# Kernel tuning notes

Measured on AMD Instinct MI355X. Metric: run time of the kernel, lower is better.

## Reference

```python
import jax, jax.numpy as jnp
from jax import lax
import numpy as np

# 32 branches: 14 base features + (worker,agv,box) x 2 entities x (state,task,pose)
DIMS = [10,3,2,3,2,8,6,8,6,3,2,2,1,1, 7,11,12, 7,11,12, 4,7,10, 4,7,10, 3,4,10, 3,4,10]
N_BRANCH = 32   # == len(VectorizedEmbedding.state_types)
T = 2048        # torch LSTM sees 2-D input as an unbatched sequence of length 'batch'
H = 256         # hidden_size
E = 2 * H       # bidirectional feature dim (d_model for attention)
DMAX = 12       # max per-branch input dim; inputs/weights zero-padded to this
NHEAD = 4


def setup_inputs() -> dict:
    key = jax.random.key(0)
    ks = jax.random.split(key, 16)
    s = 0.1
    x = jax.random.normal(ks[0], (N_BRANCH, T, DMAX), jnp.float32)
    mask = np.zeros((N_BRANCH, 1, DMAX), np.float32)
    for i, d in enumerate(DIMS):
        mask[i, 0, :d] = 1.0
    x = x * jnp.asarray(mask)  # zero padding -> identical math to per-branch dims
    inp = {
        'x': x,
        'w_ih_f': jax.random.normal(ks[1], (N_BRANCH, 4 * H, DMAX), jnp.float32) * s,
        'w_hh_f': jax.random.normal(ks[2], (N_BRANCH, 4 * H, H), jnp.float32) * s,
        'b_f':    jax.random.normal(ks[3], (N_BRANCH, 4 * H), jnp.float32) * s,
        'w_ih_b': jax.random.normal(ks[4], (N_BRANCH, 4 * H, DMAX), jnp.float32) * s,
        'w_hh_b': jax.random.normal(ks[5], (N_BRANCH, 4 * H, H), jnp.float32) * s,
        'b_b':    jax.random.normal(ks[6], (N_BRANCH, 4 * H), jnp.float32) * s,
        'type_emb': jax.random.normal(ks[7], (N_BRANCH, E), jnp.float32) * s,
        'wq': jax.random.normal(ks[8], (E, E), jnp.float32) * s,
        'bq': jnp.zeros((E,), jnp.float32),
        'wk': jax.random.normal(ks[9], (E, E), jnp.float32) * s,
        'bk': jnp.zeros((E,), jnp.float32),
        'wv': jax.random.normal(ks[10], (E, E), jnp.float32) * s,
        'bv': jnp.zeros((E,), jnp.float32),
        'wo': jax.random.normal(ks[11], (E, E), jnp.float32) * s,
        'bo': jnp.zeros((E,), jnp.float32),
    }
    return inp


def _lstm_dir(x, w_ih, w_hh, b):
    # x: (N,T,D); w_ih: (N,4H,D); w_hh: (N,4H,H); b: (N,4H) (= b_ih + b_hh)
    xw = jnp.einsum('ntd,ngd->ntg', x, w_ih) + b[:, None, :]  # (N,T,4H)
    h0 = jnp.zeros((x.shape[0], w_hh.shape[-1]), x.dtype)

    def step(carry, xt):
        h, c = carry
        g = xt + jnp.einsum('nh,ngh->ng', h, w_hh)
        i, f, gg, o = jnp.split(g, 4, axis=-1)  # torch gate order i,f,g,o
        c = jax.nn.sigmoid(f) * c + jax.nn.sigmoid(i) * jnp.tanh(gg)
        h = jax.nn.sigmoid(o) * jnp.tanh(c)
        return (h, c), h

    _, hs = lax.scan(step, (h0, h0), jnp.swapaxes(xw, 0, 1))  # hs: (T,N,H)
    return jnp.swapaxes(hs, 0, 1)  # (N,T,H)


def _forward(x, w_ih_f, w_hh_f, b_f, w_ih_b, w_hh_b, b_b, type_emb,
             wq, bq, wk, bk, wv, bv, wo, bo):
    fwd = _lstm_dir(x, w_ih_f, w_hh_f, b_f)
    bwd = _lstm_dir(x[:, ::-1], w_ih_b, w_hh_b, b_b)[:, ::-1]
    embs = jnp.concatenate([fwd, bwd], axis=-1)      # (N,T,E)
    all_embs = jnp.swapaxes(embs, 0, 1)              # (T,N,E) == (batch, seq, d_model)

    # MultiheadAttentionGlobalHead: q = slot 0, k = inputs + type_embedding, v = inputs
    B = all_embs.shape[0]
    d = E // NHEAD
    q = all_embs[:, 0] @ wq.T + bq                   # (B,E)
    k = (all_embs + type_emb[None]) @ wk.T + bk      # (B,N,E)
    v = all_embs @ wv.T + bv                         # (B,N,E)
    qh = q.reshape(B, NHEAD, d)
    kh = k.reshape(B, N_BRANCH, NHEAD, d)
    vh = v.reshape(B, N_BRANCH, NHEAD, d)
    scores = jnp.einsum('bhd,bshd->bhs', qh, kh) / jnp.sqrt(jnp.float32(d))
    w = jax.nn.softmax(scores, axis=-1)              # (B,H,S); dropout off (eval)
    ctx = jnp.einsum('bhs,bshd->bhd', w, vh).reshape(B, E)
    out = ctx @ wo.T + bo                            # (B,E)
    attn = w.mean(axis=1)                            # (B,S) avg over heads (torch default)
    return out, attn


def reference(x, w_ih_f, w_hh_f, b_f, w_ih_b, w_hh_b, b_b, type_emb,
              wq, bq, wk, bk, wv, bv, wo, bo):
    return _forward(x, w_ih_f, w_hh_f, b_f, w_ih_b, w_hh_b, b_b, type_emb,
                    wq, bq, wk, bk, wv, bv, wo, bo)
```

## Files before the change

kernel.cpp:

```cpp
#include <hip/hip_runtime.h>

typedef _Float16 half_t;
typedef _Float16 half2_t __attribute__((ext_vector_type(2)));
typedef _Float16 half4_t __attribute__((ext_vector_type(4)));
typedef _Float16 half8_t __attribute__((ext_vector_type(8)));
typedef float    floatx4 __attribute__((ext_vector_type(4)));

#define T_SEQ 2048
#define EDIM  512

static constexpr size_t EMB_OFF = 0;
static constexpr size_t Q_OFF   = 67108864;
static constexpr size_t WQ_OFF  = Q_OFF  + 2097152;
static constexpr size_t WK_OFF  = WQ_OFF + 524288;
static constexpr size_t WV_OFF  = WK_OFF + 524288;
static constexpr size_t WO_OFF  = WV_OFF + 524288;
static constexpr size_t TE_OFF  = WO_OFF + 524288;

__device__ __forceinline__ float fdot2f(half2_t a, half2_t b, float c) {
#if __has_builtin(__builtin_amdgcn_fdot2)
  return __builtin_amdgcn_fdot2(a, b, c, false);
#else
  return c + (float)a[0] * (float)b[0] + (float)a[1] * (float)b[1];
#endif
}
__device__ __forceinline__ half2_t mkh2(float a, float b) {
  half2_t r; r[0] = (half_t)a; r[1] = (half_t)b; return r;
}
__device__ __forceinline__ half2_t h2bc(unsigned u) { return __builtin_bit_cast(half2_t, u); }
__device__ __forceinline__ unsigned h2u(half2_t h)  { return __builtin_bit_cast(unsigned, h); }
__device__ __forceinline__ float sigm(float v)  { return __builtin_amdgcn_rcpf(1.f + __expf(-v)); }
__device__ __forceinline__ float tanhf_(float v){ return __builtin_amdgcn_rcpf(1.f + __expf(-2.f * v)) * 2.f - 1.f; }

__global__ void convert_kernel(const float* __restrict__ wq, const float* __restrict__ wk,
                               const float* __restrict__ wvv, const float* __restrict__ wo,
                               const float* __restrict__ te, const float* __restrict__ x,
                               half_t* __restrict__ wq16, half_t* __restrict__ wk16,
                               half_t* __restrict__ wv16, half_t* __restrict__ wo16,
                               half_t* __restrict__ te16, half_t* __restrict__ x16) {
  int i4 = (blockIdx.x * 256 + threadIdx.x) * 4;
  const float* src; half_t* dst; int off;
  if      (i4 < 262144)     { src = wq;  dst = wq16; off = i4; }
  else if (i4 < 2 * 262144) { src = wk;  dst = wk16; off = i4 - 262144; }
  else if (i4 < 3 * 262144) { src = wvv; dst = wv16; off = i4 - 2 * 262144; }
  else if (i4 < 4 * 262144) { src = wo;  dst = wo16; off = i4 - 3 * 262144; }
  else if (i4 < 4 * 262144 + 16384) { src = te; dst = te16; off = i4 - 4 * 262144; }
  else                      { src = x;   dst = x16;  off = i4 - (4 * 262144 + 16384); }
  float4 v = *(const float4*)(src + off);
  half4_t h; h[0] = (half_t)v.x; h[1] = (half_t)v.y; h[2] = (half_t)v.z; h[3] = (half_t)v.w;
  *(half4_t*)(dst + off) = h;
}

#define HB_STRIDE 272
#define LSTM_LDS_BYTES (16 * 512 * 16 + 2 * HB_STRIDE * 2)

__global__ __launch_bounds__(512, 1)
void lstm_kernel(const half_t* __restrict__ x16,
                 const float* __restrict__ wih_f, const float* __restrict__ whh_f, const float* __restrict__ b_f,
                 const float* __restrict__ wih_b, const float* __restrict__ whh_b, const float* __restrict__ b_b,
                 half_t* __restrict__ emb) {
  extern __shared__ char smem[];
  uint4*  wtail = (uint4*)smem;
  half_t* hbuf  = (half_t*)(smem + 16 * 512 * 16);

  const int bid = blockIdx.x;
  const int n = bid >> 1, dir = bid & 1;
  const int t = threadIdx.x;
  const int j = t >> 1, hf = t & 1;
  const float* wih  = dir ? wih_b : wih_f;
  const float* whh  = dir ? whh_b : whh_f;
  const float* bias = dir ? b_b   : b_f;

  half2_t w[4][48];
  half2_t wir[2][6];
  float   bb0, bb1;

#pragma unroll
  for (int r = 0; r < 4; ++r) {
    const size_t row = (size_t)n * 1024 + r * 256 + j;
    const float4* wp = (const float4*)(whh + row * 256 + hf * 128);
#pragma unroll
    for (int c = 0; c < 24; ++c) {
      float4 w4 = wp[c];
      w[r][c * 2]     = mkh2(w4.x, w4.y);
      w[r][c * 2 + 1] = mkh2(w4.z, w4.w);
    }
#pragma unroll
    for (int c = 0; c < 4; ++c) {
      float4 a = wp[24 + 2 * c], b2 = wp[25 + 2 * c];
      uint4 u;
      u.x = h2u(mkh2(a.x, a.y));   u.y = h2u(mkh2(a.z, a.w));
      u.z = h2u(mkh2(b2.x, b2.y)); u.w = h2u(mkh2(b2.z, b2.w));
      wtail[(r * 4 + c) * 512 + t] = u;
    }
  }
  {
    const int rbase = hf * 2;
#pragma unroll
    for (int rr = 0; rr < 2; ++rr) {
      const size_t row = (size_t)n * 1024 + (rbase + rr) * 256 + j;
      const float4* ip = (const float4*)(wih + row * 12);
      float4 a = ip[0], b2 = ip[1], c4 = ip[2];
      wir[rr][0] = mkh2(a.x, a.y);  wir[rr][1] = mkh2(a.z, a.w);
      wir[rr][2] = mkh2(b2.x, b2.y); wir[rr][3] = mkh2(b2.z, b2.w);
      wir[rr][4] = mkh2(c4.x, c4.y); wir[rr][5] = mkh2(c4.z, c4.w);
    }
    bb0 = bias[(size_t)n * 1024 + (rbase + 0) * 256 + j];
    bb1 = bias[(size_t)n * 1024 + (rbase + 1) * 256 + j];
  }
  if (t < 2 * HB_STRIDE) hbuf[t] = (half_t)0.f;
  __syncthreads();

  float cst = 0.f;
  half2_t xh[6];
  {
    const int t0 = dir ? 2047 : 0;
    const uint2* xp = (const uint2*)(x16 + ((size_t)n * T_SEQ + t0) * 12);
    uint2 u0 = xp[0], u1 = xp[1], u2 = xp[2];
    xh[0] = h2bc(u0.x); xh[1] = h2bc(u0.y);
    xh[2] = h2bc(u1.x); xh[3] = h2bc(u1.y);
    xh[4] = h2bc(u2.x); xh[5] = h2bc(u2.y);
  }

#pragma unroll 1
  for (int s = 0; s < T_SEQ; ++s) {
    const int tcur = dir ? (2047 - s) : s;
    int tnext = dir ? (2046 - s) : (s + 1);
    if (s == 2047) tnext = tcur;

    float p0 = bb0, p1 = bb1;
#pragma unroll
    for (int d = 0; d < 6; ++d) {
      p0 = fdot2f(wir[0][d], xh[d], p0);
      p1 = fdot2f(wir[1][d], xh[d], p1);
    }

    {
      const uint2* xnp = (const uint2*)(x16 + ((size_t)n * T_SEQ + tnext) * 12);
      uint2 u0 = xnp[0], u1 = xnp[1], u2 = xnp[2];
      xh[0] = h2bc(u0.x); xh[1] = h2bc(u0.y);
      xh[2] = h2bc(u1.x); xh[3] = h2bc(u1.y);
      xh[4] = h2bc(u2.x); xh[5] = h2bc(u2.y);
    }

    float acc0 = hf ? 0.f : p0;
    float acc1 = hf ? 0.f : p1;
    float acc2 = hf ? p0 : 0.f;
    float acc3 = hf ? p1 : 0.f;

    const uint4* hb = (const uint4*)(hbuf + (s & 1) * HB_STRIDE) + hf * 17;
#pragma unroll
    for (int c = 0; c < 12; ++c) {
      uint4 hv = hb[c];
      half2_t h0 = h2bc(hv.x), h1 = h2bc(hv.y), h2 = h2bc(hv.z), h3 = h2bc(hv.w);
      acc0 = fdot2f(w[0][4 * c + 0], h0, acc0);
      acc0 = fdot2f(w[0][4 * c + 1], h1, acc0);
      acc0 = fdot2f(w[0][4 * c + 2], h2, acc0);
      acc0 = fdot2f(w[0][4 * c + 3], h3, acc0);
      acc1 = fdot2f(w[1][4 * c + 0], h0, acc1);
      acc1 = fdot2f(w[1][4 * c + 1], h1, acc1);
      acc1 = fdot2f(w[1][4 * c + 2], h2, acc1);
      acc1 = fdot2f(w[1][4 * c + 3], h3, acc1);
      acc2 = fdot2f(w[2][4 * c + 0], h0, acc2);
      acc2 = fdot2f(w[2][4 * c + 1], h1, acc2);
      acc2 = fdot2f(w[2][4 * c + 2], h2, acc2);
      acc2 = fdot2f(w[2][4 * c + 3], h3, acc2);
      acc3 = fdot2f(w[3][4 * c + 0], h0, acc3);
      acc3 = fdot2f(w[3][4 * c + 1], h1, acc3);
      acc3 = fdot2f(w[3][4 * c + 2], h2, acc3);
      acc3 = fdot2f(w[3][4 * c + 3], h3, acc3);
    }
#pragma unroll
    for (int c = 0; c < 4; ++c) {
      uint4 hv = hb[12 + c];
      half2_t h0 = h2bc(hv.x), h1 = h2bc(hv.y), h2 = h2bc(hv.z), h3 = h2bc(hv.w);
      uint4 w0 = wtail[(0 * 4 + c) * 512 + t];
      acc0 = fdot2f(h2bc(w0.x), h0, acc0);
      acc0 = fdot2f(h2bc(w0.y), h1, acc0);
      acc0 = fdot2f(h2bc(w0.z), h2, acc0);
      acc0 = fdot2f(h2bc(w0.w), h3, acc0);
      uint4 w1 = wtail[(1 * 4 + c) * 512 + t];
      acc1 = fdot2f(h2bc(w1.x), h0, acc1);
      acc1 = fdot2f(h2bc(w1.y), h1, acc1);
      acc1 = fdot2f(h2bc(w1.z), h2, acc1);
      acc1 = fdot2f(h2bc(w1.w), h3, acc1);
      uint4 w2 = wtail[(2 * 4 + c) * 512 + t];
      acc2 = fdot2f(h2bc(w2.x), h0, acc2);
      acc2 = fdot2f(h2bc(w2.y), h1, acc2);
      acc2 = fdot2f(h2bc(w2.z), h2, acc2);
      acc2 = fdot2f(h2bc(w2.w), h3, acc2);
      uint4 w3 = wtail[(3 * 4 + c) * 512 + t];
      acc3 = fdot2f(h2bc(w3.x), h0, acc3);
      acc3 = fdot2f(h2bc(w3.y), h1, acc3);
      acc3 = fdot2f(h2bc(w3.z), h2, acc3);
      acc3 = fdot2f(h2bc(w3.w), h3, acc3);
    }

    acc0 += __shfl_xor(acc0, 1);
    acc1 += __shfl_xor(acc1, 1);
    acc2 += __shfl_xor(acc2, 1);
    acc3 += __shfl_xor(acc3, 1);

    float si = sigm(acc0), sf = sigm(acc1), gg = tanhf_(acc2), so = sigm(acc3);
    cst = sf * cst + si * gg;
    float h = so * tanhf_(cst);
    if (!hf) {
      half_t hh = (half_t)h;
      const int pos = j + ((j >> 7) << 3);
      hbuf[((s + 1) & 1) * HB_STRIDE + pos] = hh;
      emb[((size_t)n * T_SEQ + tcur) * EDIM + dir * 256 + j] = hh;
    }
    __syncthreads();
  }
}

__global__ __launch_bounds__(256, 1)
void qproj_kernel(const half_t* __restrict__ emb, const half_t* __restrict__ wq16,
                  const float* __restrict__ bq, half_t* __restrict__ q_ws) {
  const int t0 = blockIdx.x * 32;
  const int tid = threadIdx.x;
  const int lane = tid & 63, wid = tid >> 6;
  const int col = lane & 15, grp = lane >> 4;

  floatx4 acc[2][8];
#pragma unroll
  for (int nt = 0; nt < 8; ++nt) {
    int eo = wid * 128 + nt * 16 + col;
    float b = bq[eo];
#pragma unroll
    for (int mt = 0; mt < 2; ++mt) { acc[mt][nt][0] = b; acc[mt][nt][1] = b; acc[mt][nt][2] = b; acc[mt][nt][3] = b; }
  }
  for (int kc = 0; kc < 16; ++kc) {
    const int e = kc * 32 + grp * 8;
    half8_t a[2];
#pragma unroll
    for (int mt = 0; mt < 2; ++mt) {
      int trow = t0 + mt * 16 + col;
      a[mt] = *(const half8_t*)(emb + (size_t)trow * EDIM + e);
    }
#pragma unroll
    for (int nt = 0; nt < 8; ++nt) {
      int eo = wid * 128 + nt * 16 + col;
      half8_t bf = *(const half8_t*)(wq16 + (size_t)eo * EDIM + e);
#pragma unroll
      for (int mt = 0; mt < 2; ++mt)
        acc[mt][nt] = __builtin_amdgcn_mfma_f32_16x16x32_f16(a[mt], bf, acc[mt][nt], 0, 0, 0);
    }
  }
#pragma unroll
  for (int mt = 0; mt < 2; ++mt)
#pragma unroll
    for (int nt = 0; nt < 8; ++nt)
#pragma unroll
      for (int r = 0; r < 4; ++r) {
        int trow = t0 + mt * 16 + grp * 4 + r;
        int eo = wid * 128 + nt * 16 + col;
        q_ws[(size_t)trow * EDIM + eo] = (half_t)acc[mt][nt][r];
      }
}

__global__ __launch_bounds__(256, 1)
void attn_kernel(const half_t* __restrict__ emb, const half_t* __restrict__ q_ws,
                 const half_t* __restrict__ wk16, const half_t* __restrict__ wv16,
                 const half_t* __restrict__ wo16, const half_t* __restrict__ te16,
                 const float* __restrict__ bk, const float* __restrict__ bv,
                 const float* __restrict__ bo, float* __restrict__ out) {
  __shared__ float  scores_lds[128];
  __shared__ float  w_lds[128];
  __shared__ half_t ctx_lds[512];

  const int t = blockIdx.x;
  const int tid = threadIdx.x;
  const int lane = tid & 63, wid = tid >> 6;
  const int col = lane & 15, grp = lane >> 4;

  floatx4 kacc[2][8], vacc[2][8];
#pragma unroll
  for (int nt = 0; nt < 8; ++nt) {
    int eo = wid * 128 + nt * 16 + col;
    float kb = bk[eo], vb = bv[eo];
#pragma unroll
    for (int mt = 0; mt < 2; ++mt) {
      kacc[mt][nt][0] = kb; kacc[mt][nt][1] = kb; kacc[mt][nt][2] = kb; kacc[mt][nt][3] = kb;
      vacc[mt][nt][0] = vb; vacc[mt][nt][1] = vb; vacc[mt][nt][2] = vb; vacc[mt][nt][3] = vb;
    }
  }
  for (int kc = 0; kc < 16; ++kc) {
    const int e = kc * 32 + grp * 8;
    half8_t av[2], ak[2];
#pragma unroll
    for (int mt = 0; mt < 2; ++mt) {
      int branch = mt * 16 + col;
      av[mt] = *(const half8_t*)(emb + ((size_t)branch * T_SEQ + t) * EDIM + e);
      half8_t te = *(const half8_t*)(te16 + (size_t)branch * EDIM + e);
      ak[mt] = av[mt] + te;
    }
#pragma unroll
    for (int nt = 0; nt < 8; ++nt) {
      int eo = wid * 128 + nt * 16 + col;
      half8_t bkf = *(const half8_t*)(wk16 + (size_t)eo * EDIM + e);
      half8_t bvf = *(const half8_t*)(wv16 + (size_t)eo * EDIM + e);
#pragma unroll
      for (int mt = 0; mt < 2; ++mt) {
        kacc[mt][nt] = __builtin_amdgcn_mfma_f32_16x16x32_f16(ak[mt], bkf, kacc[mt][nt], 0, 0, 0);
        vacc[mt][nt] = __builtin_amdgcn_mfma_f32_16x16x32_f16(av[mt], bvf, vacc[mt][nt], 0, 0, 0);
      }
    }
  }

  float spart[8];
#pragma unroll
  for (int i = 0; i < 8; ++i) spart[i] = 0.f;
#pragma unroll
  for (int nt = 0; nt < 8; ++nt) {
    int eo = wid * 128 + nt * 16 + col;
    float qf = (float)q_ws[(size_t)t * EDIM + eo];
#pragma unroll
    for (int mt = 0; mt < 2; ++mt)
#pragma unroll
      for (int r = 0; r < 4; ++r)
        spart[mt * 4 + r] += qf * kacc[mt][nt][r];
  }
#pragma unroll
  for (int i = 0; i < 8; ++i) {
    float v = spart[i];
    v += __shfl_xor(v, 1); v += __shfl_xor(v, 2); v += __shfl_xor(v, 4); v += __shfl_xor(v, 8);
    spart[i] = v;
  }
  const float scale = 0.08838834764831845f;
  if (col == 0) {
#pragma unroll
    for (int mt = 0; mt < 2; ++mt)
#pragma unroll
      for (int r = 0; r < 4; ++r)
        scores_lds[wid * 32 + mt * 16 + grp * 4 + r] = spart[mt * 4 + r] * scale;
  }
  float sc = scores_lds[wid * 32 + (lane & 31)];
  float m = sc;
  m = fmaxf(m, __shfl_xor(m, 1));  m = fmaxf(m, __shfl_xor(m, 2));
  m = fmaxf(m, __shfl_xor(m, 4));  m = fmaxf(m, __shfl_xor(m, 8));
  m = fmaxf(m, __shfl_xor(m, 16));
  float ex = __expf(sc - m);
  float sm = ex;
  sm += __shfl_xor(sm, 1); sm += __shfl_xor(sm, 2); sm += __shfl_xor(sm, 4);
  sm += __shfl_xor(sm, 8); sm += __shfl_xor(sm, 16);
  float wn = ex * __builtin_amdgcn_rcpf(sm);
  if (lane < 32) w_lds[wid * 32 + lane] = wn;

  float wb[8];
#pragma unroll
  for (int mt = 0; mt < 2; ++mt)
#pragma unroll
    for (int r = 0; r < 4; ++r)
      wb[mt * 4 + r] = w_lds[wid * 32 + mt * 16 + grp * 4 + r];
#pragma unroll
  for (int nt = 0; nt < 8; ++nt) {
    float cx = 0.f;
#pragma unroll
    for (int mt = 0; mt < 2; ++mt)
#pragma unroll
      for (int r = 0; r < 4; ++r)
        cx += wb[mt * 4 + r] * vacc[mt][nt][r];
    cx += __shfl_xor(cx, 16);
    cx += __shfl_xor(cx, 32);
    float cxh = __shfl_xor(cx, 1);
    if ((lane < 16) && ((lane & 1) == 0))
      *(half2_t*)(ctx_lds + wid * 128 + nt * 16 + lane) = mkh2(cx, cxh);
  }
  __syncthreads();

  if (tid < 32) {
    float a = 0.25f * (w_lds[tid] + w_lds[32 + tid] + w_lds[64 + tid] + w_lds[96 + tid]);
    out[1048576 + (size_t)t * 32 + tid] = a;
  }
  const int eo2 = tid * 2;
  float o0 = bo[eo2], o1 = bo[eo2 + 1];
  const uint4* cl = (const uint4*)ctx_lds;
  const half_t* wrow0 = wo16 + (size_t)eo2 * EDIM;
  const half_t* wrow1 = wrow0 + EDIM;
#pragma unroll 8
  for (int c = 0; c < 64; ++c) {
    uint4 cv = cl[c];
    uint4 w0 = *(const uint4*)(wrow0 + c * 8);
    uint4 w1 = *(const uint4*)(wrow1 + c * 8);
    half2_t c0 = h2bc(cv.x), c1 = h2bc(cv.y), c2 = h2bc(cv.z), c3 = h2bc(cv.w);
    o0 = fdot2f(h2bc(w0.x), c0, o0);
    o0 = fdot2f(h2bc(w0.y), c1, o0);
    o0 = fdot2f(h2bc(w0.z), c2, o0);
    o0 = fdot2f(h2bc(w0.w), c3, o0);
    o1 = fdot2f(h2bc(w1.x), c0, o1);
    o1 = fdot2f(h2bc(w1.y), c1, o1);
    o1 = fdot2f(h2bc(w1.z), c2, o1);
    o1 = fdot2f(h2bc(w1.w), c3, o1);
  }
  out[(size_t)t * EDIM + eo2]     = o0;
  out[(size_t)t * EDIM + eo2 + 1] = o1;
}

extern "C" void kernel_launch(void* const* d_in, const int* in_sizes, int n_in,
                              void* d_out, int out_size, void* d_ws, size_t ws_size,
                              hipStream_t stream) {
  const float* x    = (const float*)d_in[0];
  const float* wihf = (const float*)d_in[1];
  const float* whhf = (const float*)d_in[2];
  const float* bf   = (const float*)d_in[3];
  const float* wihb = (const float*)d_in[4];
  const float* whhb = (const float*)d_in[5];
  const float* bbv  = (const float*)d_in[6];
  const float* te   = (const float*)d_in[7];
  const float* wq   = (const float*)d_in[8];
  const float* bq   = (const float*)d_in[9];
  const float* wk   = (const float*)d_in[10];
  const float* bk   = (const float*)d_in[11];
  const float* wvv  = (const float*)d_in[12];
  const float* bv   = (const float*)d_in[13];
  const float* wo   = (const float*)d_in[14];
  const float* bo   = (const float*)d_in[15];
  float* out = (float*)d_out;

  char* ws = (char*)d_ws;
  half_t* emb  = (half_t*)(ws + EMB_OFF);
  half_t* q_ws = (half_t*)(ws + Q_OFF);
  half_t* x16  = (half_t*)(ws + Q_OFF);
  half_t* wq16 = (half_t*)(ws + WQ_OFF);
  half_t* wk16 = (half_t*)(ws + WK_OFF);
  half_t* wv16 = (half_t*)(ws + WV_OFF);
  half_t* wo16 = (half_t*)(ws + WO_OFF);
  half_t* te16 = (half_t*)(ws + TE_OFF);

  convert_kernel<<<1808, 256, 0, stream>>>(wq, wk, wvv, wo, te, x,
                                           wq16, wk16, wv16, wo16, te16, x16);

  (void)hipFuncSetAttribute((const void*)lstm_kernel,
                            hipFuncAttributeMaxDynamicSharedMemorySize, LSTM_LDS_BYTES);
  lstm_kernel<<<64, 512, LSTM_LDS_BYTES, stream>>>(x16, wihf, whhf, bf, wihb, whhb, bbv, emb);

  qproj_kernel<<<64, 256, 0, stream>>>(emb, wq16, bq, q_ws);

  attn_kernel<<<2048, 256, 0, stream>>>(emb, q_ws, wk16, wv16, wo16, te16, bk, bv, bo, out);
}
```

Measured before the change: 3.667 ms.

## Move LSTM recurrent matvec onto MFMA with warp-specialized input projection

The per-step W_hh·h product is now done with 16x16x32 f16 MFMA instructions instead of per-thread fdot2 chains. Most weight fragments stay in registers and the last two K-chunks come from LDS. Gate pre-activations are staged through LDS, where 256 threads apply the cell update while the other 256 compute the next step's input projection and prefetch x. This trades the scalar dot-product cost for matrix-core throughput, but it wastes 15/16 of each MFMA because every A row holds the same h vector. It also adds a second barrier per step and rounds the gate sums to fp16.

```diff
diff --git a/kernel.cpp b/kernel.cpp
--- a/kernel.cpp
+++ b/kernel.cpp
@@ -51,8 +51,7 @@
   *(half4_t*)(dst + off) = h;
 }
 
-#define HB_STRIDE 272
-#define LSTM_LDS_BYTES (16 * 512 * 16 + 2 * HB_STRIDE * 2)
+#define LSTM_LDS_BYTES (131072 + 24576 + 4096 + 2048 + 1024)
 
 __global__ __launch_bounds__(512, 1)
 void lstm_kernel(const half_t* __restrict__ x16,
@@ -60,155 +59,179 @@
                  const float* __restrict__ wih_b, const float* __restrict__ whh_b, const float* __restrict__ b_b,
                  half_t* __restrict__ emb) {
   extern __shared__ char smem[];
-  uint4*  wtail = (uint4*)smem;
-  half_t* hbuf  = (half_t*)(smem + 16 * 512 * 16);
-
-  const int bid = blockIdx.x;
-  const int n = bid >> 1, dir = bid & 1;
-  const int t = threadIdx.x;
-  const int j = t >> 1, hf = t & 1;
+  char*   whh_lds  = smem;
+  half_t* wih_lds  = (half_t*)(smem + 131072);
+  half_t* xw_lds   = (half_t*)(smem + 131072 + 24576);
+  half_t* gate_lds = (half_t*)(smem + 131072 + 24576 + 4096);
+  half_t* hbuf     = (half_t*)(smem + 131072 + 24576 + 4096 + 2048);
+
+  const int bid = blockIdx.x, br = bid >> 1, dir = bid & 1;
+  const int tid = threadIdx.x, lane = tid & 63, w = tid >> 6;
+  const int cl = lane & 15, kg = lane >> 4;
+
   const float* wih  = dir ? wih_b : wih_f;
   const float* whh  = dir ? whh_b : whh_f;
   const float* bias = dir ? b_b   : b_f;
 
-  half2_t w[4][48];
-  half2_t wir[2][6];
-  float   bb0, bb1;
-
-#pragma unroll
-  for (int r = 0; r < 4; ++r) {
-    const size_t row = (size_t)n * 1024 + r * 256 + j;
-    const float4* wp = (const float4*)(whh + row * 256 + hf * 128);
-#pragma unroll
-    for (int c = 0; c < 24; ++c) {
-      float4 w4 = wp[c];
-      w[r][c * 2]     = mkh2(w4.x, w4.y);
-      w[r][c * 2 + 1] = mkh2(w4.z, w4.w);
-    }
-#pragma unroll
-    for (int c = 0; c < 4; ++c) {
-      float4 a = wp[24 + 2 * c], b2 = wp[25 + 2 * c];
-      uint4 u;
-      u.x = h2u(mkh2(a.x, a.y));   u.y = h2u(mkh2(a.z, a.w));
-      u.z = h2u(mkh2(b2.x, b2.y)); u.w = h2u(mkh2(b2.z, b2.w));
-      wtail[(r * 4 + c) * 512 + t] = u;
-    }
-  }
-  {
-    const int rbase = hf * 2;
-#pragma unroll
-    for (int rr = 0; rr < 2; ++rr) {
-      const size_t row = (size_t)n * 1024 + (rbase + rr) * 256 + j;
-      const float4* ip = (const float4*)(wih + row * 12);
-      float4 a = ip[0], b2 = ip[1], c4 = ip[2];
-      wir[rr][0] = mkh2(a.x, a.y);  wir[rr][1] = mkh2(a.z, a.w);
-      wir[rr][2] = mkh2(b2.x, b2.y); wir[rr][3] = mkh2(b2.z, b2.w);
-      wir[rr][4] = mkh2(c4.x, c4.y); wir[rr][5] = mkh2(c4.z, c4.w);
-    }
-    bb0 = bias[(size_t)n * 1024 + (rbase + 0) * 256 + j];
-    bb1 = bias[(size_t)n * 1024 + (rbase + 1) * 256 + j];
-  }
-  if (t < 2 * HB_STRIDE) hbuf[t] = (half_t)0.f;
-  __syncthreads();
-
-  float cst = 0.f;
-  half2_t xh[6];
+  half8_t bfrag[6][8];
+#pragma unroll
+  for (int kc = 0; kc < 6; ++kc)
+#pragma unroll
+    for (int nt = 0; nt < 8; ++nt) {
+      const float* s = whh + ((size_t)br * 1024 + w * 128 + nt * 16 + cl) * 256 + kc * 32 + kg * 8;
+      float4 a = *(const float4*)s, b = *(const float4*)(s + 4);
+      half8_t h8;
+      h8[0] = (half_t)a.x; h8[1] = (half_t)a.y; h8[2] = (half_t)a.z; h8[3] = (half_t)a.w;
+      h8[4] = (half_t)b.x; h8[5] = (half_t)b.y; h8[6] = (half_t)b.z; h8[7] = (half_t)b.w;
+      bfrag[kc][nt] = h8;
+    }
+#pragma unroll
+  for (int c = 0; c < 2; ++c)
+#pragma unroll
+    for (int nt = 0; nt < 8; ++nt) {
+      const float* s = whh + ((size_t)br * 1024 + w * 128 + nt * 16 + cl) * 256 + (6 + c) * 32 + kg * 8;
+      float4 a = *(const float4*)s, b = *(const float4*)(s + 4);
+      half8_t h8;
+      h8[0] = (half_t)a.x; h8[1] = (half_t)a.y; h8[2] = (half_t)a.z; h8[3] = (half_t)a.w;
+      h8[4] = (half_t)b.x; h8[5] = (half_t)b.y; h8[6] = (half_t)b.z; h8[7] = (half_t)b.w;
+      *(half8_t*)(whh_lds + (((w * 2 + c) * 8 + nt) * 64 + lane) * 16) = h8;
+    }
+#pragma unroll
+  for (int rr = 0; rr < 2; ++rr) {
+    const int row = tid * 2 + rr;
+    const float* s = wih + ((size_t)br * 1024 + row) * 12;
+    half_t* d = wih_lds + row * 12;
+#pragma unroll
+    for (int q = 0; q < 3; ++q) {
+      float4 v = *(const float4*)(s + q * 4);
+      half4_t h4; h4[0] = (half_t)v.x; h4[1] = (half_t)v.y; h4[2] = (half_t)v.z; h4[3] = (half_t)v.w;
+      *(half4_t*)(d + q * 4) = h4;
+    }
+  }
+  const int tt = (tid >= 256) ? (tid - 256) : 0;
+  float bias4[4];
+#pragma unroll
+  for (int r = 0; r < 4; ++r) bias4[r] = bias[(size_t)br * 1024 + tt * 4 + r];
+
+  if (tid < 256) { hbuf[tid] = (half_t)0.f; hbuf[256 + tid] = (half_t)0.f; }
+
+  unsigned xs0, xs1, xs2, xs3, xs4, xs5;
   {
     const int t0 = dir ? 2047 : 0;
-    const uint2* xp = (const uint2*)(x16 + ((size_t)n * T_SEQ + t0) * 12);
-    uint2 u0 = xp[0], u1 = xp[1], u2 = xp[2];
-    xh[0] = h2bc(u0.x); xh[1] = h2bc(u0.y);
-    xh[2] = h2bc(u1.x); xh[3] = h2bc(u1.y);
-    xh[4] = h2bc(u2.x); xh[5] = h2bc(u2.y);
-  }
+    const unsigned* xp = (const unsigned*)(x16 + ((size_t)br * T_SEQ + t0) * 12);
+    xs0 = __builtin_amdgcn_readfirstlane(xp[0]); xs1 = __builtin_amdgcn_readfirstlane(xp[1]);
+    xs2 = __builtin_amdgcn_readfirstlane(xp[2]); xs3 = __builtin_amdgcn_readfirstlane(xp[3]);
+    xs4 = __builtin_amdgcn_readfirstlane(xp[4]); xs5 = __builtin_amdgcn_readfirstlane(xp[5]);
+  }
+  __syncthreads();
+
+  if (tid >= 256) {
+    float p[4] = { bias4[0], bias4[1], bias4[2], bias4[3] };
+    half2_t xp2[6] = { h2bc(xs0), h2bc(xs1), h2bc(xs2), h2bc(xs3), h2bc(xs4), h2bc(xs5) };
+#pragma unroll
+    for (int r = 0; r < 4; ++r) {
+      const half_t* wr = wih_lds + (tt * 4 + r) * 12;
+#pragma unroll
+      for (int q = 0; q < 3; ++q) {
+        uint2 u = *(const uint2*)(wr + q * 4);
+        p[r] = fdot2f(h2bc(u.x), xp2[2 * q], p[r]);
+        p[r] = fdot2f(h2bc(u.y), xp2[2 * q + 1], p[r]);
+      }
+    }
+#pragma unroll
+    for (int r = 0; r < 4; ++r) {
+      const int nn = tt * 4 + r;
+      xw_lds[((nn >> 7) * 16 + (nn & 15)) * 8 + ((nn >> 4) & 7)] = (half_t)p[r];
+    }
+  }
+  unsigned xd0, xd1, xd2, xd3, xd4, xd5;
+  {
+    const int q1 = dir ? 2046 : 1, q2 = dir ? 2045 : 2;
+    const unsigned* p1 = (const unsigned*)(x16 + ((size_t)br * T_SEQ + q1) * 12);
+    const unsigned* p2 = (const unsigned*)(x16 + ((size_t)br * T_SEQ + q2) * 12);
+    xs0 = __builtin_amdgcn_readfirstlane(p1[0]); xs1 = __builtin_amdgcn_readfirstlane(p1[1]);
+    xs2 = __builtin_amdgcn_readfirstlane(p1[2]); xs3 = __builtin_amdgcn_readfirstlane(p1[3]);
+    xs4 = __builtin_amdgcn_readfirstlane(p1[4]); xs5 = __builtin_amdgcn_readfirstlane(p1[5]);
+    xd0 = p2[0]; xd1 = p2[1]; xd2 = p2[2]; xd3 = p2[3]; xd4 = p2[4]; xd5 = p2[5];
+  }
+  __syncthreads();
+
+  floatx4 acc[8];
+#pragma unroll
+  for (int nt = 0; nt < 8; ++nt) acc[nt] = floatx4{0.f, 0.f, 0.f, 0.f};
+  float cst = 0.f;
 
 #pragma unroll 1
   for (int s = 0; s < T_SEQ; ++s) {
-    const int tcur = dir ? (2047 - s) : s;
-    int tnext = dir ? (2046 - s) : (s + 1);
-    if (s == 2047) tnext = tcur;
-
-    float p0 = bb0, p1 = bb1;
-#pragma unroll
-    for (int d = 0; d < 6; ++d) {
-      p0 = fdot2f(wir[0][d], xh[d], p0);
-      p1 = fdot2f(wir[1][d], xh[d], p1);
-    }
-
-    {
-      const uint2* xnp = (const uint2*)(x16 + ((size_t)n * T_SEQ + tnext) * 12);
-      uint2 u0 = xnp[0], u1 = xnp[1], u2 = xnp[2];
-      xh[0] = h2bc(u0.x); xh[1] = h2bc(u0.y);
-      xh[2] = h2bc(u1.x); xh[3] = h2bc(u1.y);
-      xh[4] = h2bc(u2.x); xh[5] = h2bc(u2.y);
-    }
-
-    float acc0 = hf ? 0.f : p0;
-    float acc1 = hf ? 0.f : p1;
-    float acc2 = hf ? p0 : 0.f;
-    float acc3 = hf ? p1 : 0.f;
-
-    const uint4* hb = (const uint4*)(hbuf + (s & 1) * HB_STRIDE) + hf * 17;
-#pragma unroll
-    for (int c = 0; c < 12; ++c) {
-      uint4 hv = hb[c];
-      half2_t h0 = h2bc(hv.x), h1 = h2bc(hv.y), h2 = h2bc(hv.z), h3 = h2bc(hv.w);
-      acc0 = fdot2f(w[0][4 * c + 0], h0, acc0);
-      acc0 = fdot2f(w[0][4 * c + 1], h1, acc0);
-      acc0 = fdot2f(w[0][4 * c + 2], h2, acc0);
-      acc0 = fdot2f(w[0][4 * c + 3], h3, acc0);
-      acc1 = fdot2f(w[1][4 * c + 0], h0, acc1);
-      acc1 = fdot2f(w[1][4 * c + 1], h1, acc1);
-      acc1 = fdot2f(w[1][4 * c + 2], h2, acc1);
-      acc1 = fdot2f(w[1][4 * c + 3], h3, acc1);
-      acc2 = fdot2f(w[2][4 * c + 0], h0, acc2);
-      acc2 = fdot2f(w[2][4 * c + 1], h1, acc2);
-      acc2 = fdot2f(w[2][4 * c + 2], h2, acc2);
-      acc2 = fdot2f(w[2][4 * c + 3], h3, acc2);
-      acc3 = fdot2f(w[3][4 * c + 0], h0, acc3);
-      acc3 = fdot2f(w[3][4 * c + 1], h1, acc3);
-      acc3 = fdot2f(w[3][4 * c + 2], h2, acc3);
-      acc3 = fdot2f(w[3][4 * c + 3], h3, acc3);
-    }
-#pragma unroll
-    for (int c = 0; c < 4; ++c) {
-      uint4 hv = hb[12 + c];
-      half2_t h0 = h2bc(hv.x), h1 = h2bc(hv.y), h2 = h2bc(hv.z), h3 = h2bc(hv.w);
-      uint4 w0 = wtail[(0 * 4 + c) * 512 + t];
-      acc0 = fdot2f(h2bc(w0.x), h0, acc0);
-      acc0 = fdot2f(h2bc(w0.y), h1, acc0);
-      acc0 = fdot2f(h2bc(w0.z), h2, acc0);
-      acc0 = fdot2f(h2bc(w0.w), h3, acc0);
-      uint4 w1 = wtail[(1 * 4 + c) * 512 + t];
-      acc1 = fdot2f(h2bc(w1.x), h0, acc1);
-      acc1 = fdot2f(h2bc(w1.y), h1, acc1);
-      acc1 = fdot2f(h2bc(w1.z), h2, acc1);
-      acc1 = fdot2f(h2bc(w1.w), h3, acc1);
-      uint4 w2 = wtail[(2 * 4 + c) * 512 + t];
-      acc2 = fdot2f(h2bc(w2.x), h0, acc2);
-      acc2 = fdot2f(h2bc(w2.y), h1, acc2);
-      acc2 = fdot2f(h2bc(w2.z), h2, acc2);
-      acc2 = fdot2f(h2bc(w2.w), h3, acc2);
-      uint4 w3 = wtail[(3 * 4 + c) * 512 + t];
-      acc3 = fdot2f(h2bc(w3.x), h0, acc3);
-      acc3 = fdot2f(h2bc(w3.y), h1, acc3);
-      acc3 = fdot2f(h2bc(w3.z), h2, acc3);
-      acc3 = fdot2f(h2bc(w3.w), h3, acc3);
-    }
-
-    acc0 += __shfl_xor(acc0, 1);
-    acc1 += __shfl_xor(acc1, 1);
-    acc2 += __shfl_xor(acc2, 1);
-    acc3 += __shfl_xor(acc3, 1);
-
-    float si = sigm(acc0), sf = sigm(acc1), gg = tanhf_(acc2), so = sigm(acc3);
-    cst = sf * cst + si * gg;
-    float h = so * tanhf_(cst);
-    if (!hf) {
+    const int cur = s & 1, nxt = cur ^ 1;
+
+    half8_t xwv = *(const half8_t*)(xw_lds + cur * 1024 + (w * 16 + cl) * 8);
+#pragma unroll
+    for (int nt = 0; nt < 8; ++nt) acc[nt][0] = (float)xwv[nt];
+
+#pragma unroll
+    for (int kc = 0; kc < 6; ++kc) {
+      half8_t A = *(const half8_t*)(hbuf + cur * 256 + kc * 32 + kg * 8);
+#pragma unroll
+      for (int nt = 0; nt < 8; ++nt)
+        acc[nt] = __builtin_amdgcn_mfma_f32_16x16x32_f16(A, bfrag[kc][nt], acc[nt], 0, 0, 0);
+    }
+#pragma unroll
+    for (int c = 0; c < 2; ++c) {
+      half8_t A = *(const half8_t*)(hbuf + cur * 256 + (6 + c) * 32 + kg * 8);
+#pragma unroll
+      for (int nt = 0; nt < 8; ++nt) {
+        half8_t B = *(const half8_t*)(whh_lds + (((w * 2 + c) * 8 + nt) * 64 + lane) * 16);
+        acc[nt] = __builtin_amdgcn_mfma_f32_16x16x32_f16(A, B, acc[nt], 0, 0, 0);
+      }
+    }
+
+    if (lane < 16) {
+      half8_t g8;
+#pragma unroll
+      for (int nt = 0; nt < 8; ++nt) g8[nt] = (half_t)acc[nt][0];
+      *(half8_t*)(gate_lds + (w * 16 + cl) * 8) = g8;
+    }
+    __syncthreads();
+
+    if (tid < 256) {
+      const int n0 = tid, n1 = tid + 256, n2 = tid + 512, n3 = tid + 768;
+      float gi = (float)gate_lds[((n0 >> 7) * 16 + (n0 & 15)) * 8 + ((n0 >> 4) & 7)];
+      float gf = (float)gate_lds[((n1 >> 7) * 16 + (n1 & 15)) * 8 + ((n1 >> 4) & 7)];
+      float gg = (float)gate_lds[((n2 >> 7) * 16 + (n2 & 15)) * 8 + ((n2 >> 4) & 7)];
+      float go = (float)gate_lds[((n3 >> 7) * 16 + (n3 & 15)) * 8 + ((n3 >> 4) & 7)];
+      float si = sigm(gi), sf = sigm(gf), tg = tanhf_(gg), so = sigm(go);
+      cst = sf * cst + si * tg;
+      float h = so * tanhf_(cst);
       half_t hh = (half_t)h;
-      const int pos = j + ((j >> 7) << 3);
-      hbuf[((s + 1) & 1) * HB_STRIDE + pos] = hh;
-      emb[((size_t)n * T_SEQ + tcur) * EDIM + dir * 256 + j] = hh;
+      hbuf[nxt * 256 + tid] = hh;
+      const int tcur = dir ? (2047 - s) : s;
+      emb[((size_t)br * T_SEQ + tcur) * EDIM + dir * 256 + tid] = hh;
+    } else {
+      float p[4] = { bias4[0], bias4[1], bias4[2], bias4[3] };
+      half2_t xp2[6] = { h2bc(xs0), h2bc(xs1), h2bc(xs2), h2bc(xs3), h2bc(xs4), h2bc(xs5) };
+#pragma unroll
+      for (int r = 0; r < 4; ++r) {
+        const half_t* wr = wih_lds + (tt * 4 + r) * 12;
+#pragma unroll
+        for (int q = 0; q < 3; ++q) {
+          uint2 u = *(const uint2*)(wr + q * 4);
+          p[r] = fdot2f(h2bc(u.x), xp2[2 * q], p[r]);
+          p[r] = fdot2f(h2bc(u.y), xp2[2 * q + 1], p[r]);
+        }
+      }
+#pragma unroll
+      for (int r = 0; r < 4; ++r) {
+        const int nn = tt * 4 + r;
+        xw_lds[nxt * 1024 + ((nn >> 7) * 16 + (nn & 15)) * 8 + ((nn >> 4) & 7)] = (half_t)p[r];
+      }
+      xs0 = __builtin_amdgcn_readfirstlane(xd0); xs1 = __builtin_amdgcn_readfirstlane(xd1);
+      xs2 = __builtin_amdgcn_readfirstlane(xd2); xs3 = __builtin_amdgcn_readfirstlane(xd3);
+      xs4 = __builtin_amdgcn_readfirstlane(xd4); xs5 = __builtin_amdgcn_readfirstlane(xd5);
+      int q3 = s + 3; if (q3 > 2047) q3 = 2047;
+      const int t3 = dir ? (2047 - q3) : q3;
+      const unsigned* p3 = (const unsigned*)(x16 + ((size_t)br * T_SEQ + t3) * 12);
+      xd0 = p3[0]; xd1 = p3[1]; xd2 = p3[2]; xd3 = p3[3]; xd4 = p3[4]; xd5 = p3[5];
     }
     __syncthreads();
   }
@@ -375,12 +398,12 @@
   }
   const int eo2 = tid * 2;
   float o0 = bo[eo2], o1 = bo[eo2 + 1];
-  const uint4* cl = (const uint4*)ctx_lds;
+  const uint4* cl2 = (const uint4*)ctx_lds;
   const half_t* wrow0 = wo16 + (size_t)eo2 * EDIM;
   const half_t* wrow1 = wrow0 + EDIM;
 #pragma unroll 8
   for (int c = 0; c < 64; ++c) {
-    uint4 cv = cl[c];
+    uint4 cv = cl2[c];
     uint4 w0 = *(const uint4*)(wrow0 + c * 8);
     uint4 w1 = *(const uint4*)(wrow1 + c * 8);
     half2_t c0 = h2bc(cv.x), c1 = h2bc(cv.y), c2 = h2bc(cv.z), c3 = h2bc(cv.w);
```

Measured after the change: 4.758 ms. +29.7%, slower.

## Split LSTM recurrent dot across four threads per hidden unit, drop LDS weight tail

Applied to the files above, without the earlier changes.

The LSTM block now uses 1024 threads, with four threads per hidden unit each holding a quarter of the recurrent weights in registers. The earlier version held 3/4 of the weights in registers and streamed the remaining quarter from LDS every step. The goal is to remove that per-step LDS weight traffic and shorten each thread's serial dot-product chain. In exchange it needs a second shuffle-reduction stage and a larger block for each per-step barrier, and it raises register pressure at 1024 threads per block.

```diff
diff --git a/kernel.cpp b/kernel.cpp
--- a/kernel.cpp
+++ b/kernel.cpp
@@ -51,62 +51,46 @@
   *(half4_t*)(dst + off) = h;
 }
 
-#define HB_STRIDE 272
-#define LSTM_LDS_BYTES (16 * 512 * 16 + 2 * HB_STRIDE * 2)
-
-__global__ __launch_bounds__(512, 1)
+#define HB_STRIDE 288
+
+__global__ __launch_bounds__(1024, 1)
 void lstm_kernel(const half_t* __restrict__ x16,
                  const float* __restrict__ wih_f, const float* __restrict__ whh_f, const float* __restrict__ b_f,
                  const float* __restrict__ wih_b, const float* __restrict__ whh_b, const float* __restrict__ b_b,
                  half_t* __restrict__ emb) {
-  extern __shared__ char smem[];
-  uint4*  wtail = (uint4*)smem;
-  half_t* hbuf  = (half_t*)(smem + 16 * 512 * 16);
+  __shared__ half_t hbuf[2 * HB_STRIDE];
 
   const int bid = blockIdx.x;
   const int n = bid >> 1, dir = bid & 1;
   const int t = threadIdx.x;
-  const int j = t >> 1, hf = t & 1;
+  const int j = t >> 2, q = t & 3;
   const float* wih  = dir ? wih_b : wih_f;
   const float* whh  = dir ? whh_b : whh_f;
   const float* bias = dir ? b_b   : b_f;
 
-  half2_t w[4][48];
-  half2_t wir[2][6];
-  float   bb0, bb1;
+  half2_t w[4][32];
+  half2_t wir[6];
+  float   bb;
 
 #pragma unroll
   for (int r = 0; r < 4; ++r) {
     const size_t row = (size_t)n * 1024 + r * 256 + j;
-    const float4* wp = (const float4*)(whh + row * 256 + hf * 128);
-#pragma unroll
-    for (int c = 0; c < 24; ++c) {
+    const float4* wp = (const float4*)(whh + row * 256 + q * 64);
+#pragma unroll
+    for (int c = 0; c < 16; ++c) {
       float4 w4 = wp[c];
       w[r][c * 2]     = mkh2(w4.x, w4.y);
       w[r][c * 2 + 1] = mkh2(w4.z, w4.w);
     }
-#pragma unroll
-    for (int c = 0; c < 4; ++c) {
-      float4 a = wp[24 + 2 * c], b2 = wp[25 + 2 * c];
-      uint4 u;
-      u.x = h2u(mkh2(a.x, a.y));   u.y = h2u(mkh2(a.z, a.w));
-      u.z = h2u(mkh2(b2.x, b2.y)); u.w = h2u(mkh2(b2.z, b2.w));
-      wtail[(r * 4 + c) * 512 + t] = u;
-    }
   }
   {
-    const int rbase = hf * 2;
-#pragma unroll
-    for (int rr = 0; rr < 2; ++rr) {
-      const size_t row = (size_t)n * 1024 + (rbase + rr) * 256 + j;
-      const float4* ip = (const float4*)(wih + row * 12);
-      float4 a = ip[0], b2 = ip[1], c4 = ip[2];
-      wir[rr][0] = mkh2(a.x, a.y);  wir[rr][1] = mkh2(a.z, a.w);
-      wir[rr][2] = mkh2(b2.x, b2.y); wir[rr][3] = mkh2(b2.z, b2.w);
-      wir[rr][4] = mkh2(c4.x, c4.y); wir[rr][5] = mkh2(c4.z, c4.w);
-    }
-    bb0 = bias[(size_t)n * 1024 + (rbase + 0) * 256 + j];
-    bb1 = bias[(size_t)n * 1024 + (rbase + 1) * 256 + j];
+    const size_t row = (size_t)n * 1024 + q * 256 + j;
+    const float4* ip = (const float4*)(wih + row * 12);
+    float4 a = ip[0], b2 = ip[1], c4 = ip[2];
+    wir[0] = mkh2(a.x, a.y);   wir[1] = mkh2(a.z, a.w);
+    wir[2] = mkh2(b2.x, b2.y); wir[3] = mkh2(b2.z, b2.w);
+    wir[4] = mkh2(c4.x, c4.y); wir[5] = mkh2(c4.z, c4.w);
+    bb = bias[row];
   }
   if (t < 2 * HB_STRIDE) hbuf[t] = (half_t)0.f;
   __syncthreads();
@@ -128,12 +112,9 @@
     int tnext = dir ? (2046 - s) : (s + 1);
     if (s == 2047) tnext = tcur;
 
-    float p0 = bb0, p1 = bb1;
-#pragma unroll
-    for (int d = 0; d < 6; ++d) {
-      p0 = fdot2f(wir[0][d], xh[d], p0);
-      p1 = fdot2f(wir[1][d], xh[d], p1);
-    }
+    float p = bb;
+#pragma unroll
+    for (int d = 0; d < 6; ++d) p = fdot2f(wir[d], xh[d], p);
 
     {
       const uint2* xnp = (const uint2*)(x16 + ((size_t)n * T_SEQ + tnext) * 12);
@@ -143,14 +124,14 @@
       xh[4] = h2bc(u2.x); xh[5] = h2bc(u2.y);
     }
 
-    float acc0 = hf ? 0.f : p0;
-    float acc1 = hf ? 0.f : p1;
-    float acc2 = hf ? p0 : 0.f;
-    float acc3 = hf ? p1 : 0.f;
-
-    const uint4* hb = (const uint4*)(hbuf + (s & 1) * HB_STRIDE) + hf * 17;
-#pragma unroll
-    for (int c = 0; c < 12; ++c) {
+    float acc0 = (q == 0) ? p : 0.f;
+    float acc1 = (q == 1) ? p : 0.f;
+    float acc2 = (q == 2) ? p : 0.f;
+    float acc3 = (q == 3) ? p : 0.f;
+
+    const uint4* hb = (const uint4*)(hbuf + (s & 1) * HB_STRIDE + q * 72);
+#pragma unroll
+    for (int c = 0; c < 8; ++c) {
       uint4 hv = hb[c];
       half2_t h0 = h2bc(hv.x), h1 = h2bc(hv.y), h2 = h2bc(hv.z), h3 = h2bc(hv.w);
       acc0 = fdot2f(w[0][4 * c + 0], h0, acc0);
@@ -170,44 +151,18 @@
       acc3 = fdot2f(w[3][4 * c + 2], h2, acc3);
       acc3 = fdot2f(w[3][4 * c + 3], h3, acc3);
     }
-#pragma unroll
-    for (int c = 0; c < 4; ++c) {
-      uint4 hv = hb[12 + c];
-      half2_t h0 = h2bc(hv.x), h1 = h2bc(hv.y), h2 = h2bc(hv.z), h3 = h2bc(hv.w);
-      uint4 w0 = wtail[(0 * 4 + c) * 512 + t];
-      acc0 = fdot2f(h2bc(w0.x), h0, acc0);
-      acc0 = fdot2f(h2bc(w0.y), h1, acc0);
-      acc0 = fdot2f(h2bc(w0.z), h2, acc0);
-      acc0 = fdot2f(h2bc(w0.w), h3, acc0);
-      uint4 w1 = wtail[(1 * 4 + c) * 512 + t];
-      acc1 = fdot2f(h2bc(w1.x), h0, acc1);
-      acc1 = fdot2f(h2bc(w1.y), h1, acc1);
-      acc1 = fdot2f(h2bc(w1.z), h2, acc1);
-      acc1 = fdot2f(h2bc(w1.w), h3, acc1);
-      uint4 w2 = wtail[(2 * 4 + c) * 512 + t];
-      acc2 = fdot2f(h2bc(w2.x), h0, acc2);
-      acc2 = fdot2f(h2bc(w2.y), h1, acc2);
-      acc2 = fdot2f(h2bc(w2.z), h2, acc2);
-      acc2 = fdot2f(h2bc(w2.w), h3, acc2);
-      uint4 w3 = wtail[(3 * 4 + c) * 512 + t];
-      acc3 = fdot2f(h2bc(w3.x), h0, acc3);
-      acc3 = fdot2f(h2bc(w3.y), h1, acc3);
-      acc3 = fdot2f(h2bc(w3.z), h2, acc3);
-      acc3 = fdot2f(h2bc(w3.w), h3, acc3);
-    }
-
-    acc0 += __shfl_xor(acc0, 1);
-    acc1 += __shfl_xor(acc1, 1);
-    acc2 += __shfl_xor(acc2, 1);
-    acc3 += __shfl_xor(acc3, 1);
+
+    acc0 += __shfl_xor(acc0, 1); acc0 += __shfl_xor(acc0, 2);
+    acc1 += __shfl_xor(acc1, 1); acc1 += __shfl_xor(acc1, 2);
+    acc2 += __shfl_xor(acc2, 1); acc2 += __shfl_xor(acc2, 2);
+    acc3 += __shfl_xor(acc3, 1); acc3 += __shfl_xor(acc3, 2);
 
     float si = sigm(acc0), sf = sigm(acc1), gg = tanhf_(acc2), so = sigm(acc3);
     cst = sf * cst + si * gg;
     float h = so * tanhf_(cst);
-    if (!hf) {
+    if (q == 0) {
       half_t hh = (half_t)h;
-      const int pos = j + ((j >> 7) << 3);
-      hbuf[((s + 1) & 1) * HB_STRIDE + pos] = hh;
+      hbuf[((s + 1) & 1) * HB_STRIDE + (j >> 6) * 72 + (j & 63)] = hh;
       emb[((size_t)n * T_SEQ + tcur) * EDIM + dir * 256 + j] = hh;
     }
     __syncthreads();
@@ -375,12 +330,12 @@
   }
   const int eo2 = tid * 2;
   float o0 = bo[eo2], o1 = bo[eo2 + 1];
-  const uint4* cl = (const uint4*)ctx_lds;
+  const uint4* cl2 = (const uint4*)ctx_lds;
   const half_t* wrow0 = wo16 + (size_t)eo2 * EDIM;
   const half_t* wrow1 = wrow0 + EDIM;
 #pragma unroll 8
   for (int c = 0; c < 64; ++c) {
-    uint4 cv = cl[c];
+    uint4 cv = cl2[c];
     uint4 w0 = *(const uint4*)(wrow0 + c * 8);
     uint4 w1 = *(const uint4*)(wrow1 + c * 8);
     half2_t c0 = h2bc(cv.x), c1 = h2bc(cv.y), c2 = h2bc(cv.z), c3 = h2bc(cv.w);
@@ -431,9 +386,7 @@
   convert_kernel<<<1808, 256, 0, stream>>>(wq, wk, wvv, wo, te, x,
                                            wq16, wk16, wv16, wo16, te16, x16);
 
-  (void)hipFuncSetAttribute((const void*)lstm_kernel,
-                            hipFuncAttributeMaxDynamicSharedMemorySize, LSTM_LDS_BYTES);
-  lstm_kernel<<<64, 512, LSTM_LDS_BYTES, stream>>>(x16, wihf, whhf, bf, wihb, whhb, bbv, emb);
+  lstm_kernel<<<64, 1024, 0, stream>>>(x16, wihf, whhf, bf, wihb, whhb, bbv, emb);
 
   qproj_kernel<<<64, 256, 0, stream>>>(emb, wq16, bq, q_ws);
 
```

After: 6.821 ms. 1.86x slower.

## Stash most recurrent LSTM weights in AGPRs, shrink arch-VGPR weight set

Applied to the files above, without the earlier changes.

Moves the bulk of the per-thread recurrent weight slice out of architectural VGPRs into accumulation registers (AGPRs) via inline v_accvgpr_write/read, keeping only 16 half2 per gate in VGPRs. The LDS tail grows from 16 to 19 uint4 slots per thread, holding the remainder. The aim is to relieve VGPR pressure and spills so more weights stay on-chip. The cost is an extra accvgpr_read instruction per fdot2 operand on the critical serial step path.

```diff
diff --git a/kernel.cpp b/kernel.cpp
--- a/kernel.cpp
+++ b/kernel.cpp
@@ -31,6 +31,17 @@
 __device__ __forceinline__ unsigned h2u(half2_t h)  { return __builtin_bit_cast(unsigned, h); }
 __device__ __forceinline__ float sigm(float v)  { return __builtin_amdgcn_rcpf(1.f + __expf(-v)); }
 __device__ __forceinline__ float tanhf_(float v){ return __builtin_amdgcn_rcpf(1.f + __expf(-2.f * v)) * 2.f - 1.f; }
+
+__device__ __forceinline__ unsigned ag_write(unsigned v) {
+  unsigned a;
+  asm volatile("v_accvgpr_write_b32 %0, %1" : "=a"(a) : "v"(v));
+  return a;
+}
+__device__ __forceinline__ half2_t ag_read(unsigned a) {
+  unsigned v;
+  asm volatile("v_accvgpr_read_b32 %0, %1" : "=v"(v) : "a"(a));
+  return h2bc(v);
+}
 
 __global__ void convert_kernel(const float* __restrict__ wq, const float* __restrict__ wk,
                                const float* __restrict__ wvv, const float* __restrict__ wo,
@@ -52,7 +63,7 @@
 }
 
 #define HB_STRIDE 272
-#define LSTM_LDS_BYTES (16 * 512 * 16 + 2 * HB_STRIDE * 2)
+#define LSTM_LDS_BYTES (19 * 512 * 16 + 2 * HB_STRIDE * 2)
 
 __global__ __launch_bounds__(512, 1)
 void lstm_kernel(const half_t* __restrict__ x16,
@@ -60,8 +71,8 @@
                  const float* __restrict__ wih_b, const float* __restrict__ whh_b, const float* __restrict__ b_b,
                  half_t* __restrict__ emb) {
   extern __shared__ char smem[];
-  uint4*  wtail = (uint4*)smem;
-  half_t* hbuf  = (half_t*)(smem + 16 * 512 * 16);
+  uint4*  wt   = (uint4*)smem;
+  half_t* hbuf = (half_t*)(smem + 19 * 512 * 16);
 
   const int bid = blockIdx.x;
   const int n = bid >> 1, dir = bid & 1;
@@ -71,27 +82,40 @@
   const float* whh  = dir ? whh_b : whh_f;
   const float* bias = dir ? b_b   : b_f;
 
-  half2_t w[4][48];
-  half2_t wir[2][6];
-  float   bb0, bb1;
+  half2_t  w[4][16];
+  unsigned wag[4][32];
+  half2_t  wir[2][6];
+  float    bb0, bb1;
 
 #pragma unroll
   for (int r = 0; r < 4; ++r) {
     const size_t row = (size_t)n * 1024 + r * 256 + j;
     const float4* wp = (const float4*)(whh + row * 256 + hf * 128);
-#pragma unroll
-    for (int c = 0; c < 24; ++c) {
-      float4 w4 = wp[c];
-      w[r][c * 2]     = mkh2(w4.x, w4.y);
-      w[r][c * 2 + 1] = mkh2(w4.z, w4.w);
-    }
-#pragma unroll
-    for (int c = 0; c < 4; ++c) {
-      float4 a = wp[24 + 2 * c], b2 = wp[25 + 2 * c];
-      uint4 u;
-      u.x = h2u(mkh2(a.x, a.y));   u.y = h2u(mkh2(a.z, a.w));
-      u.z = h2u(mkh2(b2.x, b2.y)); u.w = h2u(mkh2(b2.z, b2.w));
-      wtail[(r * 4 + c) * 512 + t] = u;
+    const int nag = (r == 3) ? 8 : 7;
+    const int nl  = 12 - nag;
+#pragma unroll
+    for (int f = 0; f < 8; ++f) {
+      float4 v = wp[f];
+      w[r][2 * f]     = mkh2(v.x, v.y);
+      w[r][2 * f + 1] = mkh2(v.z, v.w);
+    }
+#pragma unroll
+    for (int f = 0; f < 16; ++f) {
+      if (f < 2 * nag) {
+        float4 v = wp[8 + f];
+        wag[r][2 * f]     = ag_write(h2u(mkh2(v.x, v.y)));
+        wag[r][2 * f + 1] = ag_write(h2u(mkh2(v.z, v.w)));
+      }
+    }
+#pragma unroll
+    for (int cc = 0; cc < 5; ++cc) {
+      if (cc < nl) {
+        float4 a = wp[8 + 2 * nag + 2 * cc], b2 = wp[9 + 2 * nag + 2 * cc];
+        uint4 u;
+        u.x = h2u(mkh2(a.x, a.y));   u.y = h2u(mkh2(a.z, a.w));
+        u.z = h2u(mkh2(b2.x, b2.y)); u.w = h2u(mkh2(b2.z, b2.w));
+        wt[((r < 3 ? r * 5 : 15) + cc) * 512 + t] = u;
+      }
     }
   }
   {
@@ -101,7 +125,7 @@
       const size_t row = (size_t)n * 1024 + (rbase + rr) * 256 + j;
       const float4* ip = (const float4*)(wih + row * 12);
       float4 a = ip[0], b2 = ip[1], c4 = ip[2];
-      wir[rr][0] = mkh2(a.x, a.y);  wir[rr][1] = mkh2(a.z, a.w);
+      wir[rr][0] = mkh2(a.x, a.y);   wir[rr][1] = mkh2(a.z, a.w);
       wir[rr][2] = mkh2(b2.x, b2.y); wir[rr][3] = mkh2(b2.z, b2.w);
       wir[rr][4] = mkh2(c4.x, c4.y); wir[rr][5] = mkh2(c4.z, c4.w);
     }
@@ -134,7 +158,6 @@
       p0 = fdot2f(wir[0][d], xh[d], p0);
       p1 = fdot2f(wir[1][d], xh[d], p1);
     }
-
     {
       const uint2* xnp = (const uint2*)(x16 + ((size_t)n * T_SEQ + tnext) * 12);
       uint2 u0 = xnp[0], u1 = xnp[1], u2 = xnp[2];
@@ -143,65 +166,48 @@
       xh[4] = h2bc(u2.x); xh[5] = h2bc(u2.y);
     }
 
-    float acc0 = hf ? 0.f : p0;
-    float acc1 = hf ? 0.f : p1;
-    float acc2 = hf ? p0 : 0.f;
-    float acc3 = hf ? p1 : 0.f;
+    float acc[4];
+    acc[0] = hf ? 0.f : p0;
+    acc[1] = hf ? 0.f : p1;
+    acc[2] = hf ? p0 : 0.f;
+    acc[3] = hf ? p1 : 0.f;
 
     const uint4* hb = (const uint4*)(hbuf + (s & 1) * HB_STRIDE) + hf * 17;
 #pragma unroll
-    for (int c = 0; c < 12; ++c) {
+    for (int c = 0; c < 16; ++c) {
       uint4 hv = hb[c];
       half2_t h0 = h2bc(hv.x), h1 = h2bc(hv.y), h2 = h2bc(hv.z), h3 = h2bc(hv.w);
-      acc0 = fdot2f(w[0][4 * c + 0], h0, acc0);
-      acc0 = fdot2f(w[0][4 * c + 1], h1, acc0);
-      acc0 = fdot2f(w[0][4 * c + 2], h2, acc0);
-      acc0 = fdot2f(w[0][4 * c + 3], h3, acc0);
-      acc1 = fdot2f(w[1][4 * c + 0], h0, acc1);
-      acc1 = fdot2f(w[1][4 * c + 1], h1, acc1);
-      acc1 = fdot2f(w[1][4 * c + 2], h2, acc1);
-      acc1 = fdot2f(w[1][4 * c + 3], h3, acc1);
-      acc2 = fdot2f(w[2][4 * c + 0], h0, acc2);
-      acc2 = fdot2f(w[2][4 * c + 1], h1, acc2);
-      acc2 = fdot2f(w[2][4 * c + 2], h2, acc2);
-      acc2 = fdot2f(w[2][4 * c + 3], h3, acc2);
-      acc3 = fdot2f(w[3][4 * c + 0], h0, acc3);
-      acc3 = fdot2f(w[3][4 * c + 1], h1, acc3);
-      acc3 = fdot2f(w[3][4 * c + 2], h2, acc3);
-      acc3 = fdot2f(w[3][4 * c + 3], h3, acc3);
-    }
-#pragma unroll
-    for (int c = 0; c < 4; ++c) {
-      uint4 hv = hb[12 + c];
-      half2_t h0 = h2bc(hv.x), h1 = h2bc(hv.y), h2 = h2bc(hv.z), h3 = h2bc(hv.w);
-      uint4 w0 = wtail[(0 * 4 + c) * 512 + t];
-      acc0 = fdot2f(h2bc(w0.x), h0, acc0);
-      acc0 = fdot2f(h2bc(w0.y), h1, acc0);
-      acc0 = fdot2f(h2bc(w0.z), h2, acc0);
-      acc0 = fdot2f(h2bc(w0.w), h3, acc0);
-      uint4 w1 = wtail[(1 * 4 + c) * 512 + t];
-      acc1 = fdot2f(h2bc(w1.x), h0, acc1);
-      acc1 = fdot2f(h2bc(w1.y), h1, acc1);
-      acc1 = fdot2f(h2bc(w1.z), h2, acc1);
-      acc1 = fdot2f(h2bc(w1.w), h3, acc1);
-      uint4 w2 = wtail[(2 * 4 + c) * 512 + t];
-      acc2 = fdot2f(h2bc(w2.x), h0, acc2);
-      acc2 = fdot2f(h2bc(w2.y), h1, acc2);
-      acc2 = fdot2f(h2bc(w2.z), h2, acc2);
-      acc2 = fdot2f(h2bc(w2.w), h3, acc2);
-      uint4 w3 = wtail[(3 * 4 + c) * 512 + t];
-      acc3 = fdot2f(h2bc(w3.x), h0, acc3);
-      acc3 = fdot2f(h2bc(w3.y), h1, acc3);
-      acc3 = fdot2f(h2bc(w3.z), h2, acc3);
-      acc3 = fdot2f(h2bc(w3.w), h3, acc3);
-    }
-
-    acc0 += __shfl_xor(acc0, 1);
-    acc1 += __shfl_xor(acc1, 1);
-    acc2 += __shfl_xor(acc2, 1);
-    acc3 += __shfl_xor(acc3, 1);
-
-    float si = sigm(acc0), sf = sigm(acc1), gg = tanhf_(acc2), so = sigm(acc3);
+#pragma unroll
+      for (int r = 0; r < 4; ++r) {
+        const int nag = (r == 3) ? 8 : 7;
+        if (c < 4) {
+          acc[r] = fdot2f(w[r][4 * c + 0], h0, acc[r]);
+          acc[r] = fdot2f(w[r][4 * c + 1], h1, acc[r]);
+          acc[r] = fdot2f(w[r][4 * c + 2], h2, acc[r]);
+          acc[r] = fdot2f(w[r][4 * c + 3], h3, acc[r]);
+        } else if (c < 4 + nag) {
+          const int bse = (c - 4) * 4;
+          acc[r] = fdot2f(ag_read(wag[r][bse + 0]), h0, acc[r]);
+          acc[r] = fdot2f(ag_read(wag[r][bse + 1]), h1, acc[r]);
+          acc[r] = fdot2f(ag_read(wag[r][bse + 2]), h2, acc[r]);
+          acc[r] = fdot2f(ag_read(wag[r][bse + 3]), h3, acc[r]);
+        } else {
+          const int slot = (r < 3 ? r * 5 : 15) + (c - 4 - nag);
+          uint4 wv = wt[slot * 512 + t];
+          acc[r] = fdot2f(h2bc(wv.x), h0, acc[r]);
+          acc[r] = fdot2f(h2bc(wv.y), h1, acc[r]);
+          acc[r] = fdot2f(h2bc(wv.z), h2, acc[r]);
+          acc[r] = fdot2f(h2bc(wv.w), h3, acc[r]);
+        }
+      }
+    }
+
+    acc[0] += __shfl_xor(acc[0], 1);
+    acc[1] += __shfl_xor(acc[1], 1);
+    acc[2] += __shfl_xor(acc[2], 1);
+    acc[3] += __shfl_xor(acc[3], 1);
+
+    float si = sigm(acc[0]), sf = sigm(acc[1]), gg = tanhf_(acc[2]), so = sigm(acc[3]);
     cst = sf * cst + si * gg;
     float h = so * tanhf_(cst);
     if (!hf) {
@@ -375,12 +381,12 @@
   }
   const int eo2 = tid * 2;
   float o0 = bo[eo2], o1 = bo[eo2 + 1];
-  const uint4* cl = (const uint4*)ctx_lds;
+  const uint4* cl2 = (const uint4*)ctx_lds;
   const half_t* wrow0 = wo16 + (size_t)eo2 * EDIM;
   const half_t* wrow1 = wrow0 + EDIM;
 #pragma unroll 8
   for (int c = 0; c < 64; ++c) {
-    uint4 cv = cl[c];
+    uint4 cv = cl2[c];
     uint4 w0 = *(const uint4*)(wrow0 + c * 8);
     uint4 w1 = *(const uint4*)(wrow1 + c * 8);
     half2_t c0 = h2bc(cv.x), c1 = h2bc(cv.y), c2 = h2bc(cv.z), c3 = h2bc(cv.w);
```

After: 4.606 ms. 1.26x slower.
